# Kernel tuning notes

Measured on AMD Instinct MI355X. Metric: run time of the kernel, lower is better.

Reference implementation:

```python
import math
import jax, jax.numpy as jnp
import numpy as np

SQ = 2048   # sequence length (hard-coded in source views)
B = 1       # batch (input_[:, 0, :] in QKVLinear)
H = 2048    # HIDDEN_SIZE
NH = 16     # NUM_HEADS
HD = 128    # head dim


def setup_inputs() -> dict:
    key = jax.random.key(0)
    ks = jax.random.split(key, 8)
    hidden_states = jax.random.normal(ks[0], (SQ, B, H), dtype=jnp.float32)
    # causal mask: True = masked (upper triangle, strictly above diagonal)
    attention_mask = jnp.triu(jnp.ones((SQ, SQ), dtype=bool), k=1)[None, None]
    qkv_w = jax.random.normal(ks[1], (3 * H, H), dtype=jnp.float32) * 0.02
    qkv_b = jax.random.normal(ks[2], (3 * H,), dtype=jnp.float32) * 0.02
    # SVD rotation matrices (approximately norm-preserving random matrices)
    svd_token = jax.random.normal(ks[3], (H, H), dtype=jnp.float32) / math.sqrt(H)
    svd_qk = jax.random.normal(ks[4], (NH, HD, HD), dtype=jnp.float32) / math.sqrt(HD)
    svd_vlin = jax.random.normal(ks[5], (NH, HD, HD), dtype=jnp.float32) / math.sqrt(HD)
    dense_w = jax.random.normal(ks[6], (NH, HD, H), dtype=jnp.float32) * 0.02
    dense_b = jax.random.normal(ks[7], (H,), dtype=jnp.float32) * 0.02
    return {
        "hidden_states": hidden_states,
        "attention_mask": attention_mask,
        "qkv_w": qkv_w,
        "qkv_b": qkv_b,
        "svd_token": svd_token,
        "svd_qk": svd_qk,
        "svd_vlin": svd_vlin,
        "dense_w": dense_w,
        "dense_b": dense_b,
    }


def reference(hidden_states, attention_mask, qkv_w, qkv_b, svd_token,
              svd_qk, svd_vlin, dense_w, dense_b):
    # QKVLinear: project input and weight through token-SVD (drop fraction = 0 -> no zeroing)
    x = hidden_states[:, 0, :] @ svd_token                 # [sq, H]
    w = qkv_w @ svd_token                                  # [3H, H]
    mixed = x @ w.T + qkv_b                                # [sq, 3H]
    mixed = mixed.reshape(SQ, B, NH, 3 * HD)
    q, k, v = jnp.split(mixed, 3, axis=-1)                 # each [sq, b, nh, hd]

    # per-head SVD-rotated Q/K (qk_drop = 0 -> h_mask is all-False, no zeroing)
    q = jnp.einsum('sbhd,hde->sbhe', q, svd_qk)
    k = jnp.einsum('sbhd,hde->sbhe', k, svd_qk)

    # scores: baddbmm with alpha = 1/(sqrt(hd)*coeff), then softmax rescales by coeff;
    # with layer_num=1 coeff=1, masked positions end at exactly -10000.
    scale = 1.0 / math.sqrt(HD)
    scores = jnp.einsum('sbhd,tbhd->bhst', q, k) * scale   # [b, nh, sq, sq]
    scores = jnp.where(attention_mask, -10000.0, scores)
    probs = jax.nn.softmax(scores, axis=-1)                # dropout in eval mode (identity)

    # per-head SVD-rotated V (vlinear_drop = 0 -> no zeroing)
    vv = jnp.einsum('sbhd,hde->sbhe', v, svd_vlin)
    ctx = jnp.einsum('bhst,tbhe->sbhe', probs, vv).reshape(SQ, B, H)

    # AttnOutputLinear: tsr block for head h = (dense_w[h].T @ svd_vlin[h]).T = svd_vlin[h].T @ dense_w[h]
    tsr = jnp.einsum('hde,hdo->heo', svd_vlin, dense_w).reshape(H, H)
    out = ctx @ tsr + dense_b                              # [sq, b, H]
    return out
```

## Files before the change

kernel.cpp:

```cpp
#include <hip/hip_runtime.h>
#include <hip/hip_bf16.h>
#include <stdint.h>
#include <math.h>


typedef __bf16 bf16_t;
typedef __bf16 bf16x8 __attribute__((ext_vector_type(8)));
typedef __bf16 bf16x4 __attribute__((ext_vector_type(4)));
typedef float  f32x4  __attribute__((ext_vector_type(4)));

__device__ __forceinline__ void async16(const void* g, void* l) {
  __builtin_amdgcn_global_load_lds(
      (const __attribute__((address_space(1))) void*)(uintptr_t)g,
      (__attribute__((address_space(3))) void*)(uint32_t)(uintptr_t)l,
      16, 0, 0);
}

__global__ __launch_bounds__(256)
void gemm_nt128(const bf16_t* __restrict__ A, const bf16_t* __restrict__ B,
                void* __restrict__ Cv, const void* __restrict__ biasv,
                int K, int lda, int ldb, int ldc, float alpha, int flags)
{
  const int bm0 = blockIdx.y * 128;
  const int bn0 = blockIdx.x * 128;

  __shared__ bf16_t shA[8192];
  __shared__ bf16_t shB[8192];

  const int t  = threadIdx.x;
  const int w  = t >> 6;
  const int l  = t & 63;
  const int wm = (w >> 1) * 64;
  const int wn = (w & 1) * 64;
  const int r0 = l >> 2;
  const int c0 = ((l & 3) ^ ((l >> 3) & 3)) * 8;
  const int fr = l & 15;
  const int kc = l >> 4;
  const int swr = ((fr >> 1) & 3);

  f32x4 acc[4][4];
  #pragma unroll
  for (int i = 0; i < 4; ++i)
    #pragma unroll
    for (int j = 0; j < 4; ++j)
      #pragma unroll
      for (int r = 0; r < 4; ++r)
        acc[i][j][r] = 0.0f;

  for (int k0 = 0; k0 < K; k0 += 64) {
    #pragma unroll
    for (int u = 0; u < 4; ++u) {
      const int seg  = u * 4 + w;
      const int half = seg >> 3;
      const int s8   = seg & 7;
      const int row  = s8 * 16 + r0;
      const int gk   = k0 + half * 32 + c0;
      async16(A + (long long)(bm0 + row) * lda + gk, &shA[half * 4096 + s8 * 512]);
      async16(B + (long long)(bn0 + row) * ldb + gk, &shB[half * 4096 + s8 * 512]);
    }
    __builtin_amdgcn_s_waitcnt(0);
    __syncthreads();

    const int rc = (kc ^ swr) * 8;
    #pragma unroll
    for (int h = 0; h < 2; ++h) {
      bf16x8 af[4], bfv[4];
      #pragma unroll
      for (int i = 0; i < 4; ++i) {
        af[i]  = *(const bf16x8*)&shA[h * 4096 + (wm + i * 16 + fr) * 32 + rc];
        bfv[i] = *(const bf16x8*)&shB[h * 4096 + (wn + i * 16 + fr) * 32 + rc];
      }
      #pragma unroll
      for (int i = 0; i < 4; ++i)
        #pragma unroll
        for (int j = 0; j < 4; ++j)
          acc[i][j] = __builtin_amdgcn_mfma_f32_16x16x32_bf16(af[i], bfv[j], acc[i][j], 0, 0, 0);
    }
    __syncthreads();
  }

  const int cc = l & 15;
  const int rq = (l >> 4) * 4;
  bf16_t* C = (bf16_t*)Cv;
  const bf16_t* bias = (flags & 8) ? (const bf16_t*)biasv : nullptr;
  #pragma unroll
  for (int j = 0; j < 4; ++j) {
    const int col = bn0 + wn + j * 16 + cc;
    const float bv = bias ? (float)bias[col] : 0.0f;
    #pragma unroll
    for (int i = 0; i < 4; ++i)
      #pragma unroll
      for (int r = 0; r < 4; ++r) {
        const int row = bm0 + wm + i * 16 + rq + r;
        C[(long long)row * ldc + col] = (bf16_t)(acc[i][j][r] * alpha + bv);
      }
  }
}

__global__ __launch_bounds__(256)
void gemm_nt64k(const bf16_t* __restrict__ A, const bf16_t* __restrict__ B,
                void* __restrict__ Cv, const void* __restrict__ biasv,
                int K, int lda, int ldb, int ldc, float alpha, int flags)
{
  const int bm0 = blockIdx.y * 64;
  const int bn0 = blockIdx.x * 128;

  __shared__ bf16_t shA[8192];
  __shared__ bf16_t shB[16384];

  const int t  = threadIdx.x;
  const int w  = t >> 6;
  const int l  = t & 63;
  const int wm = (w >> 1) * 32;
  const int wn = (w & 1) * 64;
  const int r0 = l >> 2;
  const int c0 = ((l & 3) ^ ((l >> 3) & 3)) * 8;
  const int fr = l & 15;
  const int kc = l >> 4;
  const int swr = ((fr >> 1) & 3);

  f32x4 acc[2][4];
  #pragma unroll
  for (int i = 0; i < 2; ++i)
    #pragma unroll
    for (int j = 0; j < 4; ++j)
      #pragma unroll
      for (int r = 0; r < 4; ++r)
        acc[i][j][r] = 0.0f;

  for (int k0 = 0; k0 < K; k0 += 128) {
    #pragma unroll
    for (int u = 0; u < 4; ++u) {
      const int seg = u * 4 + w;
      const int q   = seg >> 2;
      const int s4  = seg & 3;
      async16(A + (long long)(bm0 + s4 * 16 + r0) * lda + (k0 + q * 32 + c0),
              &shA[q * 2048 + s4 * 512]);
    }
    #pragma unroll
    for (int u = 0; u < 8; ++u) {
      const int seg = u * 4 + w;
      const int q   = seg >> 3;
      const int s8  = seg & 7;
      async16(B + (long long)(bn0 + s8 * 16 + r0) * ldb + (k0 + q * 32 + c0),
              &shB[q * 4096 + s8 * 512]);
    }
    __builtin_amdgcn_s_waitcnt(0);
    __syncthreads();

    const int rc = (kc ^ swr) * 8;
    #pragma unroll
    for (int q = 0; q < 4; ++q) {
      bf16x8 af[2], bfv[4];
      #pragma unroll
      for (int i = 0; i < 2; ++i)
        af[i]  = *(const bf16x8*)&shA[q * 2048 + (wm + i * 16 + fr) * 32 + rc];
      #pragma unroll
      for (int j = 0; j < 4; ++j)
        bfv[j] = *(const bf16x8*)&shB[q * 4096 + (wn + j * 16 + fr) * 32 + rc];
      #pragma unroll
      for (int i = 0; i < 2; ++i)
        #pragma unroll
        for (int j = 0; j < 4; ++j)
          acc[i][j] = __builtin_amdgcn_mfma_f32_16x16x32_bf16(af[i], bfv[j], acc[i][j], 0, 0, 0);
    }
    __syncthreads();
  }

  const int cc = l & 15;
  const int rq = (l >> 4) * 4;
  if (flags & 4) {
    float* C = (float*)Cv;
    const float* bias = (const float*)biasv;
    #pragma unroll
    for (int j = 0; j < 4; ++j) {
      const int col = bn0 + wn + j * 16 + cc;
      const float bv = bias ? bias[col] : 0.0f;
      #pragma unroll
      for (int i = 0; i < 2; ++i)
        #pragma unroll
        for (int r = 0; r < 4; ++r) {
          const int row = bm0 + wm + i * 16 + rq + r;
          C[(long long)row * ldc + col] = acc[i][j][r] * alpha + bv;
        }
    }
  } else {
    bf16_t* C = (bf16_t*)Cv;
    #pragma unroll
    for (int j = 0; j < 4; ++j) {
      const int col = bn0 + wn + j * 16 + cc;
      #pragma unroll
      for (int i = 0; i < 2; ++i)
        #pragma unroll
        for (int r = 0; r < 4; ++r) {
          const int row = bm0 + wm + i * 16 + rq + r;
          C[(long long)row * ldc + col] = (bf16_t)(acc[i][j][r] * alpha);
        }
    }
  }
}

__global__ __launch_bounds__(256)
void gemm_mprep(const bf16_t* __restrict__ qkT, const bf16_t* __restrict__ vlT,
                const bf16_t* __restrict__ qkv_wT, const bf16_t* __restrict__ dwT,
                bf16_t* __restrict__ Wrot, bf16_t* __restrict__ tsrT,
                const bf16_t* __restrict__ stb, bf16_t* __restrict__ Mbuf)
{
  __shared__ bf16_t smem[16384];
  const int z = blockIdx.x;
  const int t  = threadIdx.x;
  const int w  = t >> 6;
  const int l  = t & 63;
  const int r0 = l >> 2;
  const int c0 = ((l & 3) ^ ((l >> 3) & 3)) * 8;
  const int fr = l & 15;
  const int kc = l >> 4;
  const int swr = ((fr >> 1) & 3);
  const int cc = l & 15;
  const int rq = (l >> 4) * 4;

  if (z < 1024) {
    const int pz = z >> 4, px = z & 15;
    const bf16_t* A;
    const bf16_t* B;
    bf16_t* C;
    int bm0, bn0;
    if (pz < 48) {
      const int h = pz / 3, p = pz - 3 * h;
      A = (p == 2 ? vlT : qkT) + h * 16384;
      B = qkv_wT + (long long)pz * 262144;
      C = Wrot + (long long)pz * 262144;
      bm0 = 0;  bn0 = px * 128;
    } else {
      const int b = pz - 48;
      A = dwT + (long long)b * 262144;
      B = vlT + b * 16384;
      C = tsrT;
      bm0 = px * 128;  bn0 = b * 128;
    }
    bf16_t* shA = smem;
    bf16_t* shB = smem + 8192;
    const int wm = (w >> 1) * 64;
    const int wn = (w & 1) * 64;
    const int arow0 = (pz < 48 ? 0 : bm0);
    const int brow0 = (pz < 48 ? bn0 : 0);

    f32x4 acc[4][4];
    #pragma unroll
    for (int i = 0; i < 4; ++i)
      #pragma unroll
      for (int j = 0; j < 4; ++j)
        #pragma unroll
        for (int r = 0; r < 4; ++r)
          acc[i][j][r] = 0.0f;

    for (int k0 = 0; k0 < 128; k0 += 64) {
      #pragma unroll
      for (int u = 0; u < 4; ++u) {
        const int seg  = u * 4 + w;
        const int half = seg >> 3;
        const int s8   = seg & 7;
        const int row  = s8 * 16 + r0;
        const int gk   = k0 + half * 32 + c0;
        async16(A + (long long)(arow0 + row) * 128 + gk, &shA[half * 4096 + s8 * 512]);
        async16(B + (long long)(brow0 + row) * 128 + gk, &shB[half * 4096 + s8 * 512]);
      }
      __builtin_amdgcn_s_waitcnt(0);
      __syncthreads();

      const int rc = (kc ^ swr) * 8;
      #pragma unroll
      for (int h = 0; h < 2; ++h) {
        bf16x8 af[4], bfv[4];
        #pragma unroll
        for (int i = 0; i < 4; ++i) {
          af[i]  = *(const bf16x8*)&shA[h * 4096 + (wm + i * 16 + fr) * 32 + rc];
          bfv[i] = *(const bf16x8*)&shB[h * 4096 + (wn + i * 16 + fr) * 32 + rc];
        }
        #pragma unroll
        for (int i = 0; i < 4; ++i)
          #pragma unroll
          for (int j = 0; j < 4; ++j)
            acc[i][j] = __builtin_amdgcn_mfma_f32_16x16x32_bf16(af[i], bfv[j], acc[i][j], 0, 0, 0);
      }
      __syncthreads();
    }

    #pragma unroll
    for (int j = 0; j < 4; ++j) {
      const int col = bn0 + wn + j * 16 + cc;
      #pragma unroll
      for (int i = 0; i < 4; ++i)
        #pragma unroll
        for (int r = 0; r < 4; ++r) {
          const int row = arow0 + wm + i * 16 + rq + r;
          C[(long long)row * 2048 + col] = (bf16_t)acc[i][j][r];
        }
    }
  } else {
    const int m = z - 1024;
    const int bm0 = (m >> 4) * 64;
    const int bn0 = (m & 15) * 128;
    bf16_t* shA = smem;
    bf16_t* shB = smem + 4096;
    const int wm = (w >> 1) * 32;
    const int wn = (w & 1) * 64;

    f32x4 acc[2][4];
    #pragma unroll
    for (int i = 0; i < 2; ++i)
      #pragma unroll
      for (int j = 0; j < 4; ++j)
        #pragma unroll
        for (int r = 0; r < 4; ++r)
          acc[i][j][r] = 0.0f;

    for (int k0 = 0; k0 < 2048; k0 += 64) {
      #pragma unroll
      for (int u = 0; u < 2; ++u) {
        const int seg  = u * 4 + w;
        const int half = seg >> 2;
        const int s4   = seg & 3;
        async16(stb + (long long)(bm0 + s4 * 16 + r0) * 2048 + (k0 + half * 32 + c0),
                &shA[half * 2048 + s4 * 512]);
      }
      #pragma unroll
      for (int u = 0; u < 4; ++u) {
        const int seg  = u * 4 + w;
        const int half = seg >> 3;
        const int s8   = seg & 7;
        async16(stb + (long long)(bn0 + s8 * 16 + r0) * 2048 + (k0 + half * 32 + c0),
                &shB[half * 4096 + s8 * 512]);
      }
      __builtin_amdgcn_s_waitcnt(0);
      __syncthreads();

      const int rc = (kc ^ swr) * 8;
      #pragma unroll
      for (int h = 0; h < 2; ++h) {
        bf16x8 af[2], bfv[4];
        #pragma unroll
        for (int i = 0; i < 2; ++i)
          af[i]  = *(const bf16x8*)&shA[h * 2048 + (wm + i * 16 + fr) * 32 + rc];
        #pragma unroll
        for (int j = 0; j < 4; ++j)
          bfv[j] = *(const bf16x8*)&shB[h * 4096 + (wn + j * 16 + fr) * 32 + rc];
        #pragma unroll
        for (int i = 0; i < 2; ++i)
          #pragma unroll
          for (int j = 0; j < 4; ++j)
            acc[i][j] = __builtin_amdgcn_mfma_f32_16x16x32_bf16(af[i], bfv[j], acc[i][j], 0, 0, 0);
      }
      __syncthreads();
    }

    #pragma unroll
    for (int j = 0; j < 4; ++j) {
      const int col = bn0 + wn + j * 16 + cc;
      #pragma unroll
      for (int i = 0; i < 2; ++i)
        #pragma unroll
        for (int r = 0; r < 4; ++r) {
          const int row = bm0 + wm + i * 16 + rq + r;
          Mbuf[(long long)row * 2048 + col] = (bf16_t)acc[i][j][r];
        }
    }
  }
}

__device__ __forceinline__ void stage128(const bf16_t* __restrict__ gp, bf16_t* lds,
                                         const long long rstride, const int w, const int l)
{
  #pragma unroll
  for (int s = 0; s < 8; ++s) {
    const int chunk = (w * 8 + s) * 64 + l;
    const int r = chunk >> 4;
    const int c = (chunk & 15) ^ (r & 7);
    async16(gp + (long long)r * rstride + c * 8, &lds[(w * 8 + s) * 512]);
  }
}

#define FK_WAIT8() do { asm volatile("s_waitcnt vmcnt(8)" ::: "memory"); \
                        __builtin_amdgcn_sched_barrier(0); } while (0)
#define FK_WAIT0() do { asm volatile("s_waitcnt vmcnt(0)" ::: "memory"); \
                        __builtin_amdgcn_sched_barrier(0); } while (0)
#define FK_BAR()   do { __builtin_amdgcn_s_barrier(); \
                        __builtin_amdgcn_sched_barrier(0); } while (0)

__global__ __launch_bounds__(256)
void flash_k(const bf16_t* __restrict__ mixed, const bf16_t* __restrict__ vT,
             bf16_t* __restrict__ ctx, float iscale)
{
  const int h  = blockIdx.x;
  const int y  = blockIdx.y;
  const int qt = (y < 16) ? (31 - y) : (y - 16);
  const int r0g = qt * 64;
  const int niter = (qt >> 1) + 1;
  const bf16_t* Qp = mixed + h * 384;
  const bf16_t* Kp = mixed + h * 384 + 128;
  const bf16_t* Vp = vT + (long long)h * 262144;

  __shared__ bf16_t sK[16384];
  __shared__ bf16_t sV[16384];
  __shared__ bf16_t sP[8192];

  const int t  = threadIdx.x;
  const int w  = t >> 6;
  const int l  = t & 63;
  const int fr = l & 15;
  const int kc = l >> 4;
  const int qrow0 = r0g + w * 16;

  bf16x8 aq[4];
  #pragma unroll
  for (int ks = 0; ks < 4; ++ks)
    aq[ks] = *(const bf16x8*)(Qp + (long long)(qrow0 + fr) * 6144 + ks * 32 + kc * 8);

  f32x4 oacc[8];
  #pragma unroll
  for (int j = 0; j < 8; ++j)
    #pragma unroll
    for (int r = 0; r < 4; ++r) oacc[j][r] = 0.0f;
  float lsum[4] = {0.f, 0.f, 0.f, 0.f};

  FK_WAIT0();

  stage128(Kp, sK, 6144, w, l);
  stage128(Vp, sV, 2048, w, l);
  FK_WAIT8();
  FK_BAR();

  for (int it = 0; it < niter; ++it) {
    const int t0 = it * 128;

    f32x4 acc[8];
    #pragma unroll
    for (int j = 0; j < 8; ++j)
      #pragma unroll
      for (int r = 0; r < 4; ++r) acc[j][r] = 0.0f;
    #pragma unroll
    for (int ks = 0; ks < 4; ++ks) {
      bf16x8 bk[8];
      #pragma unroll
      for (int j = 0; j < 8; ++j)
        bk[j] = *(const bf16x8*)&sK[(j * 16 + fr) * 128 + (((ks * 4 + kc) ^ (fr & 7)) * 8)];
      __builtin_amdgcn_s_setprio(1);
      #pragma unroll
      for (int j = 0; j < 8; ++j)
        acc[j] = __builtin_amdgcn_mfma_f32_16x16x32_bf16(aq[ks], bk[j], acc[j], 0, 0, 0);
      __builtin_amdgcn_s_setprio(0);
    }

    #pragma unroll
    for (int r = 0; r < 4; ++r) {
      const int q16 = kc * 4 + r;
      const int Rg  = qrow0 + q16;
      float rs = 0.f;
      #pragma unroll
      for (int j = 0; j < 8; ++j) {
        const float e = (t0 + j * 16 + fr <= Rg) ? __expf(acc[j][r] * iscale) : 0.0f;
        rs += e;
        sP[(w * 16 + q16) * 128 + (((j * 2 + (fr >> 3)) ^ (q16 & 7)) * 8) + (fr & 7)] = (bf16_t)e;
      }
      rs += __shfl_xor(rs, 1, 64);
      rs += __shfl_xor(rs, 2, 64);
      rs += __shfl_xor(rs, 4, 64);
      rs += __shfl_xor(rs, 8, 64);
      lsum[r] += rs;
    }

    FK_BAR();
    if (it + 1 < niter) {
      stage128(Kp + (long long)(t0 + 128) * 6144, sK, 6144, w, l);
      FK_WAIT8();
    } else {
      FK_WAIT0();
    }
    FK_BAR();

    #pragma unroll
    for (int ks = 0; ks < 4; ++ks) {
      const bf16x8 ap =
          *(const bf16x8*)&sP[(w * 16 + fr) * 128 + (((ks * 4 + kc) ^ (fr & 7)) * 8)];
      bf16x8 bv[8];
      #pragma unroll
      for (int j = 0; j < 8; ++j)
        bv[j] = *(const bf16x8*)&sV[(j * 16 + fr) * 128 + (((ks * 4 + kc) ^ (fr & 7)) * 8)];
      __builtin_amdgcn_s_setprio(1);
      #pragma unroll
      for (int j = 0; j < 8; ++j)
        oacc[j] = __builtin_amdgcn_mfma_f32_16x16x32_bf16(ap, bv[j], oacc[j], 0, 0, 0);
      __builtin_amdgcn_s_setprio(0);
    }

    if (it + 1 < niter) {
      FK_BAR();
      stage128(Vp + (t0 + 128), sV, 2048, w, l);
      FK_WAIT8();
      FK_BAR();
    }
  }

  #pragma unroll
  for (int r = 0; r < 4; ++r) {
    const float inv = 1.0f / lsum[r];
    const int rowg = qrow0 + kc * 4 + r;
    #pragma unroll
    for (int j = 0; j < 8; ++j)
      ctx[(long long)rowg * 2048 + h * 128 + j * 16 + fr] = (bf16_t)(oacc[j][r] * inv);
  }
}

__global__ __launch_bounds__(256)
void front_k(const float* __restrict__ hs, bf16_t* __restrict__ hsb,
             const float* __restrict__ svd_tok, bf16_t* __restrict__ stb,
             const float* __restrict__ svd_qk, bf16_t* __restrict__ qkT,
             const float* __restrict__ svd_vl, bf16_t* __restrict__ vlT,
             const float* __restrict__ qkv_w, bf16_t* __restrict__ qkv_wT,
             const float* __restrict__ dense_w, bf16_t* __restrict__ dwT,
             const float* __restrict__ qkv_b, bf16_t* __restrict__ brot)
{
  __shared__ bf16_t sm[32][33];
  const int z = blockIdx.x;
  const int tid = threadIdx.x;

  if (z < 2048) {
    const float* in = (z < 1024) ? hs : svd_tok;
    bf16_t* out = (z < 1024) ? hsb : stb;
    const int base = (z & 1023) * 4096 + tid * 16;
    #pragma unroll
    for (int j = 0; j < 4; ++j) {
      const f32x4 v = *(const f32x4*)(in + base + j * 4);
      bf16x4 o;
      #pragma unroll
      for (int k = 0; k < 4; ++k) o[k] = (bf16_t)v[k];
      *(bf16x4*)(out + base + j * 4) = o;
    }
  } else if (z < 2560) {
    const int zz = z - 2048;
    const int zr = zz >> 4;
    const int tile = zz & 15;
    const float* ip = (zr < 16 ? svd_qk : svd_vl) + (long long)(zr & 15) * 16384;
    bf16_t* op = (zr < 16 ? qkT : vlT) + (long long)(zr & 15) * 16384;
    const int r0 = (tile & 3) << 5;
    const int c0 = (tile >> 2) << 5;
    const int tx = tid & 31;
    const int ty = tid >> 5;
    #pragma unroll
    for (int yy = ty; yy < 32; yy += 8)
      sm[yy][tx] = (bf16_t)ip[(long long)(r0 + yy) * 128 + c0 + tx];
    __syncthreads();
    #pragma unroll
    for (int yy = ty; yy < 32; yy += 8)
      op[(long long)(c0 + yy) * 128 + r0 + tx] = sm[tx][yy];
  } else if (z < 18944) {
    const int zz = z - 2560;
    const int zb = zz >> 8;
    const int tile = zz & 255;
    const float* ip = (zb < 48) ? qkv_w + (long long)zb * 262144
                                : dense_w + (long long)(zb - 48) * 262144;
    bf16_t* op = (zb < 48) ? qkv_wT + (long long)zb * 262144
                           : dwT + (long long)(zb - 48) * 262144;
    const int r0 = (tile & 3) << 5;
    const int c0 = (tile >> 2) << 5;
    const int tx = tid & 31;
    const int ty = tid >> 5;
    #pragma unroll
    for (int yy = ty; yy < 32; yy += 8)
      sm[yy][tx] = (bf16_t)ip[(long long)(r0 + yy) * 2048 + c0 + tx];
    __syncthreads();
    #pragma unroll
    for (int yy = ty; yy < 32; yy += 8)
      op[(long long)(c0 + yy) * 128 + r0 + tx] = sm[tx][yy];
  } else {
    const int hp = (z - 18944) * 2 + (tid >> 7);
    const int h = hp / 3, p = hp % 3;
    const int e = tid & 127;
    const float* R = (p == 2 ? (const float*)svd_vl : (const float*)svd_qk) + (long long)h * 16384;
    const float* b = qkv_b + h * 384 + p * 128;
    float acc = 0.f;
    for (int d = 0; d < 128; ++d)
      acc += b[d] * R[d * 128 + e];
    brot[h * 384 + p * 128 + e] = (bf16_t)acc;
  }
}

__global__ __launch_bounds__(256)
void transpose_b2b(const bf16_t* __restrict__ in, bf16_t* __restrict__ out,
                   int R, long long zsi, int rsi, long long zso)
{
  __shared__ bf16_t sm[32][33];
  const int z  = blockIdx.z;
  const int r0 = blockIdx.x << 5;
  const int c0 = blockIdx.y << 5;
  const int tx = threadIdx.x & 31;
  const int ty = threadIdx.x >> 5;
  const bf16_t* ip = in + (long long)z * zsi;
  bf16_t* op = out + (long long)z * zso;
  #pragma unroll
  for (int yy = ty; yy < 32; yy += 8)
    sm[yy][tx] = ip[(long long)(r0 + yy) * rsi + c0 + tx];
  __syncthreads();
  #pragma unroll
  for (int yy = ty; yy < 32; yy += 8)
    op[(long long)(c0 + yy) * R + r0 + tx] = sm[tx][yy];
}

extern "C" void kernel_launch(void* const* d_in, const int* in_sizes, int n_in,
                              void* d_out, int out_size, void* d_ws, size_t ws_size,
                              hipStream_t stream)
{
  const float* hs      = (const float*)d_in[0];
  const float* qkv_w   = (const float*)d_in[2];
  const float* qkv_b   = (const float*)d_in[3];
  const float* svd_tok = (const float*)d_in[4];
  const float* svd_qk  = (const float*)d_in[5];
  const float* svd_vl  = (const float*)d_in[6];
  const float* dense_w = (const float*)d_in[7];
  const float* dense_b = (const float*)d_in[8];
  float* out = (float*)d_out;
  bf16_t* ws = (bf16_t*)d_ws;

  bf16_t* hsb    = ws;
  bf16_t* stb    = ws +  4194304LL;
  bf16_t* Mbuf   = ws +  8388608LL;
  bf16_t* x2     = ws + 12582912LL;
  bf16_t* qkv_wT = ws + 16777216LL;
  bf16_t* Wrot   = ws + 29360128LL;
  bf16_t* mixed  = ws + 41943040LL;
  bf16_t* vT     = ws + 54525952LL;
  bf16_t* ctx    = ws + 58720256LL;
  bf16_t* dwT    = ws + 62914560LL;
  bf16_t* tsrT   = ws + 67108864LL;
  bf16_t* qkT    = ws + 71303168LL;
  bf16_t* vlT    = ws + 71565312LL;
  bf16_t* brot   = ws + 71827456LL;
  if (ws_size < 71833600ULL * 2ULL) return;

  const float iscale = 0.08838834764831845f;

  front_k<<<dim3(18968), 256, 0, stream>>>(hs, hsb, svd_tok, stb,
      svd_qk, qkT, svd_vl, vlT, qkv_w, qkv_wT, dense_w, dwT, qkv_b, brot);
  gemm_mprep<<<dim3(1536), 256, 0, stream>>>(qkT, vlT, qkv_wT, dwT,
      Wrot, tsrT, stb, Mbuf);
  gemm_nt64k<<<dim3(16, 32), 256, 0, stream>>>(hsb, Mbuf, x2, nullptr,
      2048, 2048, 2048, 2048, 1.0f, 0);
  gemm_nt128<<<dim3(48, 16), 256, 0, stream>>>(x2, Wrot, mixed, brot,
      2048, 2048, 2048, 6144, 1.0f, 8);
  transpose_b2b<<<dim3(64, 4, 16), 256, 0, stream>>>(mixed + 256, vT, 2048, 384, 6144, 262144);
  flash_k<<<dim3(16, 32), 256, 0, stream>>>(mixed, vT, ctx, iscale);
  gemm_nt64k<<<dim3(16, 32), 256, 0, stream>>>(ctx, tsrT, out, dense_b,
      2048, 2048, 2048, 2048, 1.0f, 4);
}
```

Before: 376.2 us.

## Replace QKV projection GEMM with 256x256 double-buffered 8-wave pipelined kernel

Swaps the 128x128 single-buffered QKV GEMM for a 256x256-tile kernel with 512 threads, double-buffered LDS staging, interleaved prefetch of the next K slice during MFMA phases, and an XCD-aware block swizzle. The aim is more reuse per tile and less exposed global-load latency between K steps. The cost is 128KB of LDS per block and only 192 blocks, which may limit occupancy and leave CUs underused on a 256-CU part.

After: 375.2 us. About the same (-0.3%).

```diff
diff --git a/kernel.cpp b/kernel.cpp
--- a/kernel.cpp
+++ b/kernel.cpp
@@ -16,85 +16,159 @@
       16, 0, 0);
 }
 
-__global__ __launch_bounds__(256)
-void gemm_nt128(const bf16_t* __restrict__ A, const bf16_t* __restrict__ B,
-                void* __restrict__ Cv, const void* __restrict__ biasv,
-                int K, int lda, int ldb, int ldc, float alpha, int flags)
-{
-  const int bm0 = blockIdx.y * 128;
-  const int bn0 = blockIdx.x * 128;
-
-  __shared__ bf16_t shA[8192];
-  __shared__ bf16_t shB[8192];
+#define FK_WAIT8() do { asm volatile("s_waitcnt vmcnt(8)" ::: "memory"); \
+                        __builtin_amdgcn_sched_barrier(0); } while (0)
+#define FK_WAIT4() do { asm volatile("s_waitcnt vmcnt(4)" ::: "memory"); \
+                        __builtin_amdgcn_sched_barrier(0); } while (0)
+#define FK_WAIT0() do { asm volatile("s_waitcnt vmcnt(0)" ::: "memory"); \
+                        __builtin_amdgcn_sched_barrier(0); } while (0)
+#define FK_BAR()   do { __builtin_amdgcn_s_barrier(); \
+                        __builtin_amdgcn_sched_barrier(0); } while (0)
+
+__device__ __forceinline__ void stage_half8(const bf16_t* __restrict__ P, int ld,
+                                            int row0, int k0, bf16_t* lds,
+                                            int w, int l)
+{
+  #pragma unroll
+  for (int h = 0; h < 2; ++h) {
+    const int r = h * 64 + w * 8 + (l >> 3);
+    const int c = (l & 7) ^ (l >> 3);
+    async16(P + (long long)(row0 + r) * ld + k0 + c * 8,
+            lds + h * 4096 + w * 512);
+  }
+}
+
+#define G8_READ_A(IH)                                                          \
+  { _Pragma("unroll") for (int ii = 0; ii < 4; ++ii) {                         \
+      _Pragma("unroll") for (int ks = 0; ks < 2; ++ks) {                       \
+        const int rr = wmB + (IH) * 64 + ii * 16 + fr;                         \
+        af[ii][ks] = *(const bf16x8*)&cA[rr * 64 + (((ks * 4 + kc) ^ (rr & 7)) * 8)]; \
+      } } }
+
+#define G8_READ_B(JH)                                                          \
+  { _Pragma("unroll") for (int jj = 0; jj < 2; ++jj) {                         \
+      _Pragma("unroll") for (int ks = 0; ks < 2; ++ks) {                       \
+        const int rr = wnB + (JH) * 32 + jj * 16 + fr;                         \
+        bfv[jj][ks] = *(const bf16x8*)&cB[rr * 64 + (((ks * 4 + kc) ^ (rr & 7)) * 8)]; \
+      } } }
+
+#define G8_MFMA(IH, JH)                                                        \
+  { __builtin_amdgcn_s_setprio(1);                                             \
+    _Pragma("unroll") for (int ks = 0; ks < 2; ++ks) {                         \
+      _Pragma("unroll") for (int ii = 0; ii < 4; ++ii) {                       \
+        _Pragma("unroll") for (int jj = 0; jj < 2; ++jj) {                     \
+          acc[(IH) * 4 + ii][(JH) * 2 + jj] =                                  \
+            __builtin_amdgcn_mfma_f32_16x16x32_bf16(af[ii][ks], bfv[jj][ks],   \
+                acc[(IH) * 4 + ii][(JH) * 2 + jj], 0, 0, 0);                   \
+        } } }                                                                  \
+    __builtin_amdgcn_s_setprio(0); }
+
+__global__ __launch_bounds__(512, 2)
+void gemm8p(const bf16_t* __restrict__ A, const bf16_t* __restrict__ B,
+            bf16_t* __restrict__ C, const bf16_t* __restrict__ bias,
+            int K, int lda, int ldb, int ldc, int nbx)
+{
+  const int nwg = (int)gridDim.x;
+  const int id  = (int)blockIdx.x;
+  const int cpx = nwg >> 3;
+  const int swz = (id & 7) * cpx + (id >> 3);
+  const int by  = swz / nbx;
+  const int bx  = swz - by * nbx;
+  const int bm0 = by * 256;
+  const int bn0 = bx * 256;
+
+  __shared__ bf16_t sA[2][16384];
+  __shared__ bf16_t sB[2][16384];
 
   const int t  = threadIdx.x;
   const int w  = t >> 6;
   const int l  = t & 63;
-  const int wm = (w >> 1) * 64;
-  const int wn = (w & 1) * 64;
-  const int r0 = l >> 2;
-  const int c0 = ((l & 3) ^ ((l >> 3) & 3)) * 8;
   const int fr = l & 15;
   const int kc = l >> 4;
-  const int swr = ((fr >> 1) & 3);
-
-  f32x4 acc[4][4];
-  #pragma unroll
-  for (int i = 0; i < 4; ++i)
+  const int wmB = (w >> 2) * 128;
+  const int wnB = (w & 3) * 64;
+
+  float bvv[2][2];
+  #pragma unroll
+  for (int JH = 0; JH < 2; ++JH)
+    #pragma unroll
+    for (int jj = 0; jj < 2; ++jj)
+      bvv[JH][jj] = (float)bias[bn0 + wnB + JH * 32 + jj * 16 + fr];
+
+  f32x4 acc[8][4];
+  #pragma unroll
+  for (int i = 0; i < 8; ++i)
     #pragma unroll
     for (int j = 0; j < 4; ++j)
       #pragma unroll
-      for (int r = 0; r < 4; ++r)
-        acc[i][j][r] = 0.0f;
-
-  for (int k0 = 0; k0 < K; k0 += 64) {
-    #pragma unroll
-    for (int u = 0; u < 4; ++u) {
-      const int seg  = u * 4 + w;
-      const int half = seg >> 3;
-      const int s8   = seg & 7;
-      const int row  = s8 * 16 + r0;
-      const int gk   = k0 + half * 32 + c0;
-      async16(A + (long long)(bm0 + row) * lda + gk, &shA[half * 4096 + s8 * 512]);
-      async16(B + (long long)(bn0 + row) * ldb + gk, &shB[half * 4096 + s8 * 512]);
-    }
-    __builtin_amdgcn_s_waitcnt(0);
-    __syncthreads();
-
-    const int rc = (kc ^ swr) * 8;
-    #pragma unroll
-    for (int h = 0; h < 2; ++h) {
-      bf16x8 af[4], bfv[4];
-      #pragma unroll
-      for (int i = 0; i < 4; ++i) {
-        af[i]  = *(const bf16x8*)&shA[h * 4096 + (wm + i * 16 + fr) * 32 + rc];
-        bfv[i] = *(const bf16x8*)&shB[h * 4096 + (wn + i * 16 + fr) * 32 + rc];
-      }
-      #pragma unroll
-      for (int i = 0; i < 4; ++i)
-        #pragma unroll
-        for (int j = 0; j < 4; ++j)
-          acc[i][j] = __builtin_amdgcn_mfma_f32_16x16x32_bf16(af[i], bfv[j], acc[i][j], 0, 0, 0);
-    }
-    __syncthreads();
-  }
-
-  const int cc = l & 15;
-  const int rq = (l >> 4) * 4;
-  bf16_t* C = (bf16_t*)Cv;
-  const bf16_t* bias = (flags & 8) ? (const bf16_t*)biasv : nullptr;
-  #pragma unroll
-  for (int j = 0; j < 4; ++j) {
-    const int col = bn0 + wn + j * 16 + cc;
-    const float bv = bias ? (float)bias[col] : 0.0f;
-    #pragma unroll
-    for (int i = 0; i < 4; ++i)
-      #pragma unroll
-      for (int r = 0; r < 4; ++r) {
-        const int row = bm0 + wm + i * 16 + rq + r;
-        C[(long long)row * ldc + col] = (bf16_t)(acc[i][j][r] * alpha + bv);
-      }
-  }
+      for (int r = 0; r < 4; ++r) acc[i][j][r] = 0.0f;
+
+  const int nk = K >> 6;
+
+  stage_half8(A, lda, bm0,       0, &sA[0][0],    w, l);
+  stage_half8(A, lda, bm0 + 128, 0, &sA[0][8192], w, l);
+  stage_half8(B, ldb, bn0,       0, &sB[0][0],    w, l);
+  stage_half8(B, ldb, bn0 + 128, 0, &sB[0][8192], w, l);
+
+  for (int m = 0; m < nk; ++m) {
+    const int b = m & 1;
+    const bf16_t* cA = sA[b];
+    const bf16_t* cB = sB[b];
+    const int k1 = (m + 1) << 6;
+    const bool pf = (m + 1 < nk);
+    bf16x8 af[4][2], bfv[2][2];
+
+    if (pf) {
+      stage_half8(A, lda, bm0,       k1, &sA[b ^ 1][0],    w, l);
+      stage_half8(A, lda, bm0 + 128, k1, &sA[b ^ 1][8192], w, l);
+      FK_WAIT4();
+    } else {
+      FK_WAIT0();
+    }
+    FK_BAR();
+    G8_READ_A(0)
+    G8_READ_B(0)
+    G8_MFMA(0, 0)
+    FK_BAR();
+
+    G8_READ_B(1)
+    if (pf) {
+      stage_half8(B, ldb, bn0,       k1, &sB[b ^ 1][0],    w, l);
+      stage_half8(B, ldb, bn0 + 128, k1, &sB[b ^ 1][8192], w, l);
+    }
+    FK_BAR();
+    G8_MFMA(0, 1)
+    FK_BAR();
+
+    G8_READ_A(1)
+    G8_READ_B(0)
+    FK_BAR();
+    G8_MFMA(1, 0)
+    FK_BAR();
+
+    G8_READ_B(1)
+    FK_BAR();
+    G8_MFMA(1, 1)
+    FK_BAR();
+  }
+
+  #pragma unroll
+  for (int JH = 0; JH < 2; ++JH)
+    #pragma unroll
+    for (int jj = 0; jj < 2; ++jj) {
+      const int col = bn0 + wnB + JH * 32 + jj * 16 + fr;
+      const float bv = bvv[JH][jj];
+      #pragma unroll
+      for (int IH = 0; IH < 2; ++IH)
+        #pragma unroll
+        for (int ii = 0; ii < 4; ++ii)
+          #pragma unroll
+          for (int r = 0; r < 4; ++r) {
+            const int row = bm0 + wmB + IH * 64 + ii * 16 + kc * 4 + r;
+            C[(long long)row * ldc + col] =
+                (bf16_t)(acc[IH * 4 + ii][JH * 2 + jj][r] + bv);
+          }
+    }
 }
 
 __global__ __launch_bounds__(256)
@@ -380,13 +454,6 @@
   }
 }
 
-#define FK_WAIT8() do { asm volatile("s_waitcnt vmcnt(8)" ::: "memory"); \
-                        __builtin_amdgcn_sched_barrier(0); } while (0)
-#define FK_WAIT0() do { asm volatile("s_waitcnt vmcnt(0)" ::: "memory"); \
-                        __builtin_amdgcn_sched_barrier(0); } while (0)
-#define FK_BAR()   do { __builtin_amdgcn_s_barrier(); \
-                        __builtin_amdgcn_sched_barrier(0); } while (0)
-
 __global__ __launch_bounds__(256)
 void flash_k(const bf16_t* __restrict__ mixed, const bf16_t* __restrict__ vT,
              bf16_t* __restrict__ ctx, float iscale)
@@ -645,8 +712,8 @@
       Wrot, tsrT, stb, Mbuf);
   gemm_nt64k<<<dim3(16, 32), 256, 0, stream>>>(hsb, Mbuf, x2, nullptr,
       2048, 2048, 2048, 2048, 1.0f, 0);
-  gemm_nt128<<<dim3(48, 16), 256, 0, stream>>>(x2, Wrot, mixed, brot,
-      2048, 2048, 2048, 6144, 1.0f, 8);
+  gemm8p<<<dim3(192), 512, 0, stream>>>(x2, Wrot, mixed, brot,
+      2048, 2048, 2048, 6144, 24);
   transpose_b2b<<<dim3(64, 4, 16), 256, 0, stream>>>(mixed + 256, vT, 2048, 384, 6144, 262144);
   flash_k<<<dim3(16, 32), 256, 0, stream>>>(mixed, vT, ctx, iscale);
   gemm_nt64k<<<dim3(16, 32), 256, 0, stream>>>(ctx, tsrT, out, dense_b,
```

## Exploit symmetry of token Gram matrix and fuse V transpose into QKV GEMM

Applied to the files above, without the earlier changes.

The Mbuf product (svd_token times its transpose) is symmetric, so only upper-triangular 128x128 super-tiles are computed and each off-diagonal tile is mirrored through LDS into its transposed position. This cuts that GEMM's block count from 512 to 272. Separately, the QKV GEMM epilogue now stages V-column tiles in LDS and writes the transposed V directly, which removes the standalone transpose kernel launch and its extra read and write of the V slice. The cost is extra LDS traffic and scattered-write work in the epilogues, and uneven per-block work on the mirrored tiles.

After: 383.8 us. 2.0% more time.

```diff
diff --git a/kernel.cpp b/kernel.cpp
--- a/kernel.cpp
+++ b/kernel.cpp
@@ -16,16 +16,25 @@
       16, 0, 0);
 }
 
+#define FK_WAIT8() do { asm volatile("s_waitcnt vmcnt(8)" ::: "memory"); \
+                        __builtin_amdgcn_sched_barrier(0); } while (0)
+#define FK_WAIT0() do { asm volatile("s_waitcnt vmcnt(0)" ::: "memory"); \
+                        __builtin_amdgcn_sched_barrier(0); } while (0)
+#define FK_BAR()   do { __builtin_amdgcn_s_barrier(); \
+                        __builtin_amdgcn_sched_barrier(0); } while (0)
+
 __global__ __launch_bounds__(256)
 void gemm_nt128(const bf16_t* __restrict__ A, const bf16_t* __restrict__ B,
                 void* __restrict__ Cv, const void* __restrict__ biasv,
+                bf16_t* __restrict__ vT,
                 int K, int lda, int ldb, int ldc, float alpha, int flags)
 {
   const int bm0 = blockIdx.y * 128;
   const int bn0 = blockIdx.x * 128;
 
-  __shared__ bf16_t shA[8192];
-  __shared__ bf16_t shB[8192];
+  __shared__ bf16_t smem[16384];
+  bf16_t* shA = smem;
+  bf16_t* shB = smem + 8192;
 
   const int t  = threadIdx.x;
   const int w  = t >> 6;
@@ -83,17 +92,40 @@
   const int rq = (l >> 4) * 4;
   bf16_t* C = (bf16_t*)Cv;
   const bf16_t* bias = (flags & 8) ? (const bf16_t*)biasv : nullptr;
+  const bool vblk = (flags & 16) && ((blockIdx.x % 3) == 2);
   #pragma unroll
   for (int j = 0; j < 4; ++j) {
-    const int col = bn0 + wn + j * 16 + cc;
+    const int coll = wn + j * 16 + cc;
+    const int col = bn0 + coll;
     const float bv = bias ? (float)bias[col] : 0.0f;
     #pragma unroll
     for (int i = 0; i < 4; ++i)
       #pragma unroll
       for (int r = 0; r < 4; ++r) {
-        const int row = bm0 + wm + i * 16 + rq + r;
-        C[(long long)row * ldc + col] = (bf16_t)(acc[i][j][r] * alpha + bv);
-      }
+        const int rowl = wm + i * 16 + rq + r;
+        const bf16_t v = (bf16_t)(acc[i][j][r] * alpha + bv);
+        C[(long long)(bm0 + rowl) * ldc + col] = v;
+        if (vblk)
+          smem[rowl * 128 + (((coll >> 3) ^ (rowl & 15)) * 8) + (coll & 7)] = v;
+      }
+  }
+
+  if (vblk) {
+    __syncthreads();
+    const int h  = (int)blockIdx.x / 3;
+    const int e  = t >> 1;
+    const int t0 = (t & 1) * 64;
+    bf16_t* vp = vT + (long long)h * 262144 + (long long)e * 2048 + bm0 + t0;
+    #pragma unroll
+    for (int u = 0; u < 64; u += 8) {
+      bf16x8 v;
+      #pragma unroll
+      for (int q = 0; q < 8; ++q) {
+        const int r = t0 + u + q;
+        v[q] = smem[r * 128 + (((e >> 3) ^ (r & 15)) * 8) + (e & 7)];
+      }
+      *(bf16x8*)(vp + u) = v;
+    }
   }
 }
 
@@ -219,8 +251,102 @@
   const int cc = l & 15;
   const int rq = (l >> 4) * 4;
 
-  if (z < 1024) {
-    const int pz = z >> 4, px = z & 15;
+  if (z < 272) {
+    int sup = z >> 1;
+    const int h2 = z & 1;
+    int I = 0;
+    #pragma unroll 1
+    while (sup >= 16 - I) { sup -= 16 - I; ++I; }
+    const int J = I + sup;
+    const int bm0 = I * 128 + h2 * 64;
+    const int bn0 = J * 128;
+    bf16_t* shA = smem;
+    bf16_t* shB = smem + 4096;
+    const int wm = (w >> 1) * 32;
+    const int wn = (w & 1) * 64;
+
+    f32x4 acc[2][4];
+    #pragma unroll
+    for (int i = 0; i < 2; ++i)
+      #pragma unroll
+      for (int j = 0; j < 4; ++j)
+        #pragma unroll
+        for (int r = 0; r < 4; ++r)
+          acc[i][j][r] = 0.0f;
+
+    for (int k0 = 0; k0 < 2048; k0 += 64) {
+      #pragma unroll
+      for (int u = 0; u < 2; ++u) {
+        const int seg  = u * 4 + w;
+        const int half = seg >> 2;
+        const int s4   = seg & 3;
+        async16(stb + (long long)(bm0 + s4 * 16 + r0) * 2048 + (k0 + half * 32 + c0),
+                &shA[half * 2048 + s4 * 512]);
+      }
+      #pragma unroll
+      for (int u = 0; u < 4; ++u) {
+        const int seg  = u * 4 + w;
+        const int half = seg >> 3;
+        const int s8   = seg & 7;
+        async16(stb + (long long)(bn0 + s8 * 16 + r0) * 2048 + (k0 + half * 32 + c0),
+                &shB[half * 4096 + s8 * 512]);
+      }
+      __builtin_amdgcn_s_waitcnt(0);
+      __syncthreads();
+
+      const int rc = (kc ^ swr) * 8;
+      #pragma unroll
+      for (int h = 0; h < 2; ++h) {
+        bf16x8 af[2], bfv[4];
+        #pragma unroll
+        for (int i = 0; i < 2; ++i)
+          af[i]  = *(const bf16x8*)&shA[h * 2048 + (wm + i * 16 + fr) * 32 + rc];
+        #pragma unroll
+        for (int j = 0; j < 4; ++j)
+          bfv[j] = *(const bf16x8*)&shB[h * 4096 + (wn + j * 16 + fr) * 32 + rc];
+        #pragma unroll
+        for (int i = 0; i < 2; ++i)
+          #pragma unroll
+          for (int j = 0; j < 4; ++j)
+            acc[i][j] = __builtin_amdgcn_mfma_f32_16x16x32_bf16(af[i], bfv[j], acc[i][j], 0, 0, 0);
+      }
+      __syncthreads();
+    }
+
+    const bool mir = (I != J);
+    #pragma unroll
+    for (int j = 0; j < 4; ++j) {
+      const int coll = wn + j * 16 + cc;
+      #pragma unroll
+      for (int i = 0; i < 2; ++i)
+        #pragma unroll
+        for (int r = 0; r < 4; ++r) {
+          const int rowl = wm + i * 16 + rq + r;
+          const bf16_t v = (bf16_t)acc[i][j][r];
+          Mbuf[(long long)(bm0 + rowl) * 2048 + bn0 + coll] = v;
+          if (mir)
+            smem[rowl * 128 + (((coll >> 3) ^ (rowl & 15)) * 8) + (coll & 7)] = v;
+        }
+    }
+    if (mir) {
+      __syncthreads();
+      const int c  = t >> 1;
+      const int rh = (t & 1) * 32;
+      bf16_t* mp = Mbuf + (long long)(bn0 + c) * 2048 + bm0 + rh;
+      #pragma unroll
+      for (int u = 0; u < 32; u += 8) {
+        bf16x8 v;
+        #pragma unroll
+        for (int q = 0; q < 8; ++q) {
+          const int r = rh + u + q;
+          v[q] = smem[r * 128 + (((c >> 3) ^ (r & 15)) * 8) + (c & 7)];
+        }
+        *(bf16x8*)(mp + u) = v;
+      }
+    }
+  } else {
+    const int zz = z - 272;
+    const int pz = zz >> 4, px = zz & 15;
     const bf16_t* A;
     const bf16_t* B;
     bf16_t* C;
@@ -297,74 +423,6 @@
           C[(long long)row * 2048 + col] = (bf16_t)acc[i][j][r];
         }
     }
-  } else {
-    const int m = z - 1024;
-    const int bm0 = (m >> 4) * 64;
-    const int bn0 = (m & 15) * 128;
-    bf16_t* shA = smem;
-    bf16_t* shB = smem + 4096;
-    const int wm = (w >> 1) * 32;
-    const int wn = (w & 1) * 64;
-
-    f32x4 acc[2][4];
-    #pragma unroll
-    for (int i = 0; i < 2; ++i)
-      #pragma unroll
-      for (int j = 0; j < 4; ++j)
-        #pragma unroll
-        for (int r = 0; r < 4; ++r)
-          acc[i][j][r] = 0.0f;
-
-    for (int k0 = 0; k0 < 2048; k0 += 64) {
-      #pragma unroll
-      for (int u = 0; u < 2; ++u) {
-        const int seg  = u * 4 + w;
-        const int half = seg >> 2;
-        const int s4   = seg & 3;
-        async16(stb + (long long)(bm0 + s4 * 16 + r0) * 2048 + (k0 + half * 32 + c0),
-                &shA[half * 2048 + s4 * 512]);
-      }
-      #pragma unroll
-      for (int u = 0; u < 4; ++u) {
-        const int seg  = u * 4 + w;
-        const int half = seg >> 3;
-        const int s8   = seg & 7;
-        async16(stb + (long long)(bn0 + s8 * 16 + r0) * 2048 + (k0 + half * 32 + c0),
-                &shB[half * 4096 + s8 * 512]);
-      }
-      __builtin_amdgcn_s_waitcnt(0);
-      __syncthreads();
-
-      const int rc = (kc ^ swr) * 8;
-      #pragma unroll
-      for (int h = 0; h < 2; ++h) {
-        bf16x8 af[2], bfv[4];
-        #pragma unroll
-        for (int i = 0; i < 2; ++i)
-          af[i]  = *(const bf16x8*)&shA[h * 2048 + (wm + i * 16 + fr) * 32 + rc];
-        #pragma unroll
-        for (int j = 0; j < 4; ++j)
-          bfv[j] = *(const bf16x8*)&shB[h * 4096 + (wn + j * 16 + fr) * 32 + rc];
-        #pragma unroll
-        for (int i = 0; i < 2; ++i)
-          #pragma unroll
-          for (int j = 0; j < 4; ++j)
-            acc[i][j] = __builtin_amdgcn_mfma_f32_16x16x32_bf16(af[i], bfv[j], acc[i][j], 0, 0, 0);
-      }
-      __syncthreads();
-    }
-
-    #pragma unroll
-    for (int j = 0; j < 4; ++j) {
-      const int col = bn0 + wn + j * 16 + cc;
-      #pragma unroll
-      for (int i = 0; i < 2; ++i)
-        #pragma unroll
-        for (int r = 0; r < 4; ++r) {
-          const int row = bm0 + wm + i * 16 + rq + r;
-          Mbuf[(long long)row * 2048 + col] = (bf16_t)acc[i][j][r];
-        }
-    }
   }
 }
 
@@ -379,13 +437,6 @@
     async16(gp + (long long)r * rstride + c * 8, &lds[(w * 8 + s) * 512]);
   }
 }
-
-#define FK_WAIT8() do { asm volatile("s_waitcnt vmcnt(8)" ::: "memory"); \
-                        __builtin_amdgcn_sched_barrier(0); } while (0)
-#define FK_WAIT0() do { asm volatile("s_waitcnt vmcnt(0)" ::: "memory"); \
-                        __builtin_amdgcn_sched_barrier(0); } while (0)
-#define FK_BAR()   do { __builtin_amdgcn_s_barrier(); \
-                        __builtin_amdgcn_sched_barrier(0); } while (0)
 
 __global__ __launch_bounds__(256)
 void flash_k(const bf16_t* __restrict__ mixed, const bf16_t* __restrict__ vT,
@@ -583,27 +634,6 @@
       acc += b[d] * R[d * 128 + e];
     brot[h * 384 + p * 128 + e] = (bf16_t)acc;
   }
-}
-
-__global__ __launch_bounds__(256)
-void transpose_b2b(const bf16_t* __restrict__ in, bf16_t* __restrict__ out,
-                   int R, long long zsi, int rsi, long long zso)
-{
-  __shared__ bf16_t sm[32][33];
-  const int z  = blockIdx.z;
-  const int r0 = blockIdx.x << 5;
-  const int c0 = blockIdx.y << 5;
-  const int tx = threadIdx.x & 31;
-  const int ty = threadIdx.x >> 5;
-  const bf16_t* ip = in + (long long)z * zsi;
-  bf16_t* op = out + (long long)z * zso;
-  #pragma unroll
-  for (int yy = ty; yy < 32; yy += 8)
-    sm[yy][tx] = ip[(long long)(r0 + yy) * rsi + c0 + tx];
-  __syncthreads();
-  #pragma unroll
-  for (int yy = ty; yy < 32; yy += 8)
-    op[(long long)(c0 + yy) * R + r0 + tx] = sm[tx][yy];
 }
 
 extern "C" void kernel_launch(void* const* d_in, const int* in_sizes, int n_in,
@@ -641,13 +671,12 @@
 
   front_k<<<dim3(18968), 256, 0, stream>>>(hs, hsb, svd_tok, stb,
       svd_qk, qkT, svd_vl, vlT, qkv_w, qkv_wT, dense_w, dwT, qkv_b, brot);
-  gemm_mprep<<<dim3(1536), 256, 0, stream>>>(qkT, vlT, qkv_wT, dwT,
+  gemm_mprep<<<dim3(1296), 256, 0, stream>>>(qkT, vlT, qkv_wT, dwT,
       Wrot, tsrT, stb, Mbuf);
   gemm_nt64k<<<dim3(16, 32), 256, 0, stream>>>(hsb, Mbuf, x2, nullptr,
       2048, 2048, 2048, 2048, 1.0f, 0);
-  gemm_nt128<<<dim3(48, 16), 256, 0, stream>>>(x2, Wrot, mixed, brot,
-      2048, 2048, 2048, 6144, 1.0f, 8);
-  transpose_b2b<<<dim3(64, 4, 16), 256, 0, stream>>>(mixed + 256, vT, 2048, 384, 6144, 262144);
+  gemm_nt128<<<dim3(48, 16), 256, 0, stream>>>(x2, Wrot, mixed, brot, vT,
+      2048, 2048, 2048, 6144, 1.0f, 8 | 16);
   flash_k<<<dim3(16, 32), 256, 0, stream>>>(mixed, vT, ctx, iscale);
   gemm_nt64k<<<dim3(16, 32), 256, 0, stream>>>(ctx, tsrT, out, dense_b,
       2048, 2048, 2048, 2048, 1.0f, 4);
```

## Exploit symmetry of Mbuf Gram product and remap GEMM tiles per XCD

Applied to the files above, without the earlier changes.

The Mbuf block (svd_token times its own transpose) is symmetric, so only upper-triangular 128x128 tile pairs are computed, and each off-diagonal tile is mirrored through LDS with a transposed store. This cuts the Mbuf blocks from 512 to 272 and shrinks the mprep grid, and those blocks are now scheduled first. Separately, the NT GEMM kernels remap block indices so that each XCD handles a contiguous set of column tiles, aiming for better L2 reuse of the B operand. The mirrored write adds extra LDS traffic and strided global stores per block.

New measurement: 361.0 us (median of 3 runs). 4.1% less time.

```diff
diff --git a/kernel.cpp b/kernel.cpp
--- a/kernel.cpp
+++ b/kernel.cpp
@@ -16,13 +16,32 @@
       16, 0, 0);
 }
 
+#define FK_WAIT8() do { asm volatile("s_waitcnt vmcnt(8)" ::: "memory"); \
+                        __builtin_amdgcn_sched_barrier(0); } while (0)
+#define FK_WAIT0() do { asm volatile("s_waitcnt vmcnt(0)" ::: "memory"); \
+                        __builtin_amdgcn_sched_barrier(0); } while (0)
+#define FK_BAR()   do { __builtin_amdgcn_s_barrier(); \
+                        __builtin_amdgcn_sched_barrier(0); } while (0)
+
+__device__ __forceinline__ void xcd_cols(int& bx, int& by) {
+  const int nbx = (int)gridDim.x;
+  const int lin = (int)blockIdx.x + nbx * (int)blockIdx.y;
+  const int xcd = lin & 7;
+  const int idx = lin >> 3;
+  const int cpx = nbx >> 3;
+  bx = xcd * cpx + idx % cpx;
+  by = idx / cpx;
+}
+
 __global__ __launch_bounds__(256)
 void gemm_nt128(const bf16_t* __restrict__ A, const bf16_t* __restrict__ B,
                 void* __restrict__ Cv, const void* __restrict__ biasv,
                 int K, int lda, int ldb, int ldc, float alpha, int flags)
 {
-  const int bm0 = blockIdx.y * 128;
-  const int bn0 = blockIdx.x * 128;
+  int bxs, bys;
+  xcd_cols(bxs, bys);
+  const int bm0 = bys * 128;
+  const int bn0 = bxs * 128;
 
   __shared__ bf16_t shA[8192];
   __shared__ bf16_t shB[8192];
@@ -102,8 +121,10 @@
                 void* __restrict__ Cv, const void* __restrict__ biasv,
                 int K, int lda, int ldb, int ldc, float alpha, int flags)
 {
-  const int bm0 = blockIdx.y * 64;
-  const int bn0 = blockIdx.x * 128;
+  int bxs, bys;
+  xcd_cols(bxs, bys);
+  const int bm0 = bys * 64;
+  const int bn0 = bxs * 128;
 
   __shared__ bf16_t shA[8192];
   __shared__ bf16_t shB[16384];
@@ -219,8 +240,98 @@
   const int cc = l & 15;
   const int rq = (l >> 4) * 4;
 
-  if (z < 1024) {
-    const int pz = z >> 4, px = z & 15;
+  if (z < 272) {
+    int sup = z >> 1;
+    const int h2 = z & 1;
+    int I = 0;
+    #pragma unroll 1
+    while (sup >= 16 - I) { sup -= 16 - I; ++I; }
+    const int J = I + sup;
+    const int bm0 = I * 128 + h2 * 64;
+    const int bn0 = J * 128;
+    bf16_t* shA = smem;
+    bf16_t* shB = smem + 4096;
+    const int wm = (w >> 1) * 32;
+    const int wn = (w & 1) * 64;
+
+    f32x4 acc[2][4];
+    #pragma unroll
+    for (int i = 0; i < 2; ++i)
+      #pragma unroll
+      for (int j = 0; j < 4; ++j)
+        #pragma unroll
+        for (int r = 0; r < 4; ++r)
+          acc[i][j][r] = 0.0f;
+
+    for (int k0 = 0; k0 < 2048; k0 += 64) {
+      #pragma unroll
+      for (int u = 0; u < 2; ++u) {
+        const int seg  = u * 4 + w;
+        const int half = seg >> 2;
+        const int s4   = seg & 3;
+        async16(stb + (long long)(bm0 + s4 * 16 + r0) * 2048 + (k0 + half * 32 + c0),
+                &shA[half * 2048 + s4 * 512]);
+      }
+      #pragma unroll
+      for (int u = 0; u < 4; ++u) {
+        const int seg  = u * 4 + w;
+        const int half = seg >> 3;
+        const int s8   = seg & 7;
+        async16(stb + (long long)(bn0 + s8 * 16 + r0) * 2048 + (k0 + half * 32 + c0),
+                &shB[half * 4096 + s8 * 512]);
+      }
+      __builtin_amdgcn_s_waitcnt(0);
+      __syncthreads();
+
+      const int rc = (kc ^ swr) * 8;
+      #pragma unroll
+      for (int h = 0; h < 2; ++h) {
+        bf16x8 af[2], bfv[4];
+        #pragma unroll
+        for (int i = 0; i < 2; ++i)
+          af[i]  = *(const bf16x8*)&shA[h * 2048 + (wm + i * 16 + fr) * 32 + rc];
+        #pragma unroll
+        for (int j = 0; j < 4; ++j)
+          bfv[j] = *(const bf16x8*)&shB[h * 4096 + (wn + j * 16 + fr) * 32 + rc];
+        #pragma unroll
+        for (int i = 0; i < 2; ++i)
+          #pragma unroll
+          for (int j = 0; j < 4; ++j)
+            acc[i][j] = __builtin_amdgcn_mfma_f32_16x16x32_bf16(af[i], bfv[j], acc[i][j], 0, 0, 0);
+      }
+      __syncthreads();
+    }
+
+    const bool mir = (I != J);
+    #pragma unroll
+    for (int j = 0; j < 4; ++j) {
+      const int coll = wn + j * 16 + cc;
+      #pragma unroll
+      for (int i = 0; i < 2; ++i)
+        #pragma unroll
+        for (int r = 0; r < 4; ++r) {
+          const int rowl = wm + i * 16 + rq + r;
+          const bf16_t v = (bf16_t)acc[i][j][r];
+          Mbuf[(long long)(bm0 + rowl) * 2048 + bn0 + coll] = v;
+          if (mir)
+            smem[coll * 64 + (((rowl >> 3) ^ (coll & 7)) * 8) + (rowl & 7)] = v;
+        }
+    }
+    if (mir) {
+      __syncthreads();
+      const int cr  = t >> 3;
+      const int mc8 = t & 7;
+      bf16_t* mp = Mbuf + bm0 + mc8 * 8;
+      #pragma unroll
+      for (int p = 0; p < 4; ++p) {
+        const int c = p * 32 + cr;
+        const bf16x8 v = *(const bf16x8*)&smem[c * 64 + ((mc8 ^ (c & 7)) * 8)];
+        *(bf16x8*)(mp + (long long)(bn0 + c) * 2048) = v;
+      }
+    }
+  } else {
+    const int zz = z - 272;
+    const int pz = zz >> 4, px = zz & 15;
     const bf16_t* A;
     const bf16_t* B;
     bf16_t* C;
@@ -297,74 +408,6 @@
           C[(long long)row * 2048 + col] = (bf16_t)acc[i][j][r];
         }
     }
-  } else {
-    const int m = z - 1024;
-    const int bm0 = (m >> 4) * 64;
-    const int bn0 = (m & 15) * 128;
-    bf16_t* shA = smem;
-    bf16_t* shB = smem + 4096;
-    const int wm = (w >> 1) * 32;
-    const int wn = (w & 1) * 64;
-
-    f32x4 acc[2][4];
-    #pragma unroll
-    for (int i = 0; i < 2; ++i)
-      #pragma unroll
-      for (int j = 0; j < 4; ++j)
-        #pragma unroll
-        for (int r = 0; r < 4; ++r)
-          acc[i][j][r] = 0.0f;
-
-    for (int k0 = 0; k0 < 2048; k0 += 64) {
-      #pragma unroll
-      for (int u = 0; u < 2; ++u) {
-        const int seg  = u * 4 + w;
-        const int half = seg >> 2;
-        const int s4   = seg & 3;
-        async16(stb + (long long)(bm0 + s4 * 16 + r0) * 2048 + (k0 + half * 32 + c0),
-                &shA[half * 2048 + s4 * 512]);
-      }
-      #pragma unroll
-      for (int u = 0; u < 4; ++u) {
-        const int seg  = u * 4 + w;
-        const int half = seg >> 3;
-        const int s8   = seg & 7;
-        async16(stb + (long long)(bn0 + s8 * 16 + r0) * 2048 + (k0 + half * 32 + c0),
-                &shB[half * 4096 + s8 * 512]);
-      }
-      __builtin_amdgcn_s_waitcnt(0);
-      __syncthreads();
-
-      const int rc = (kc ^ swr) * 8;
-      #pragma unroll
-      for (int h = 0; h < 2; ++h) {
-        bf16x8 af[2], bfv[4];
-        #pragma unroll
-        for (int i = 0; i < 2; ++i)
-          af[i]  = *(const bf16x8*)&shA[h * 2048 + (wm + i * 16 + fr) * 32 + rc];
-        #pragma unroll
-        for (int j = 0; j < 4; ++j)
-          bfv[j] = *(const bf16x8*)&shB[h * 4096 + (wn + j * 16 + fr) * 32 + rc];
-        #pragma unroll
-        for (int i = 0; i < 2; ++i)
-          #pragma unroll
-          for (int j = 0; j < 4; ++j)
-            acc[i][j] = __builtin_amdgcn_mfma_f32_16x16x32_bf16(af[i], bfv[j], acc[i][j], 0, 0, 0);
-      }
-      __syncthreads();
-    }
-
-    #pragma unroll
-    for (int j = 0; j < 4; ++j) {
-      const int col = bn0 + wn + j * 16 + cc;
-      #pragma unroll
-      for (int i = 0; i < 2; ++i)
-        #pragma unroll
-        for (int r = 0; r < 4; ++r) {
-          const int row = bm0 + wm + i * 16 + rq + r;
-          Mbuf[(long long)row * 2048 + col] = (bf16_t)acc[i][j][r];
-        }
-    }
   }
 }
 
@@ -379,13 +422,6 @@
     async16(gp + (long long)r * rstride + c * 8, &lds[(w * 8 + s) * 512]);
   }
 }
-
-#define FK_WAIT8() do { asm volatile("s_waitcnt vmcnt(8)" ::: "memory"); \
-                        __builtin_amdgcn_sched_barrier(0); } while (0)
-#define FK_WAIT0() do { asm volatile("s_waitcnt vmcnt(0)" ::: "memory"); \
-                        __builtin_amdgcn_sched_barrier(0); } while (0)
-#define FK_BAR()   do { __builtin_amdgcn_s_barrier(); \
-                        __builtin_amdgcn_sched_barrier(0); } while (0)
 
 __global__ __launch_bounds__(256)
 void flash_k(const bf16_t* __restrict__ mixed, const bf16_t* __restrict__ vT,
@@ -641,7 +677,7 @@
 
   front_k<<<dim3(18968), 256, 0, stream>>>(hs, hsb, svd_tok, stb,
       svd_qk, qkT, svd_vl, vlT, qkv_w, qkv_wT, dense_w, dwT, qkv_b, brot);
-  gemm_mprep<<<dim3(1536), 256, 0, stream>>>(qkT, vlT, qkv_wT, dwT,
+  gemm_mprep<<<dim3(1296), 256, 0, stream>>>(qkT, vlT, qkv_wT, dwT,
       Wrot, tsrT, stb, Mbuf);
   gemm_nt64k<<<dim3(16, 32), 256, 0, stream>>>(hsb, Mbuf, x2, nullptr,
       2048, 2048, 2048, 2048, 1.0f, 0);
```
